# Kernel tuning notes

Measured on AMD Instinct MI355X. Metric: run time of the kernel, lower is better.

Reference implementation:

```python
import jax, jax.numpy as jnp
import numpy as np

G, N, E = 4, 50000, 400000   # subgraphs, nodes/graph, edges/graph
D = 128                      # num_node_feat = num_g_hid = out_g_ch
L = 3                        # num_layers
NE, AH = 8, 64               # num_expert, num_att_hid
FE = 8                       # num_edge_feat (unused by GIN conv)
LN_EPS = 1e-5


def setup_inputs() -> dict:
    key = jax.random.key(0)
    ks = jax.random.split(key, 12)
    s = 1.0 / np.sqrt(D)
    inp = {
        "decomp_x": jax.random.normal(ks[0], (G, N, D), dtype=jnp.float32),
        "decomp_edge_index": jax.random.randint(ks[1], (G, 2, E), 0, N, dtype=jnp.int32),
        "decomp_edge_attr": jax.random.normal(ks[2], (G, E, FE), dtype=jnp.float32),
        # GIN MLP params per layer: Linear(D,D) -> ReLU -> Linear(D,D), stored [in,out]
        "Ws1": jax.random.uniform(ks[3], (L, D, D), jnp.float32, -s, s),
        "bs1": jax.random.uniform(ks[4], (L, D), jnp.float32, -s, s),
        "Ws2": jax.random.uniform(ks[5], (L, D, D), jnp.float32, -s, s),
        "bs2": jax.random.uniform(ks[6], (L, D), jnp.float32, -s, s),
        "ln_g": jnp.ones((L, D), jnp.float32),
        "ln_b": jnp.zeros((L, D), jnp.float32),
        # Attention: w1 [n_hidden, v_hidden], w2 [n_expert, n_hidden]
        "att_w1": jax.random.uniform(ks[7], (AH, D), jnp.float32, -1.0 / np.sqrt(D), 1.0 / np.sqrt(D)),
        "att_w2": jax.random.uniform(ks[8], (NE, AH), jnp.float32, -1.0 / np.sqrt(AH), 1.0 / np.sqrt(AH)),
    }
    return inp


def _layer_norm(h, g, b):
    mu = jnp.mean(h, axis=-1, keepdims=True)
    var = jnp.var(h, axis=-1, keepdims=True)
    return (h - mu) * jax.lax.rsqrt(var + LN_EPS) * g + b


def _gin_graph(x, edge_index, Ws1, bs1, Ws2, bs2, ln_g, ln_b):
    # x: [N, D]; edge_index: [2, E] (src, dst)
    src, dst = edge_index[0], edge_index[1]
    for l in range(L):
        identity = x
        # GINConv (eps=0): MLP(x_i + sum_{j->i} x_j)
        agg = jax.ops.segment_sum(x[src], dst, num_segments=N)  # gather+scatter
        h = x + agg
        h = jnp.maximum(h @ Ws1[l] + bs1[l], 0.0) @ Ws2[l] + bs2[l]
        if l < L - 1:
            h = h + identity  # same dims, no projection
        x = _layer_norm(h, ln_g[l], ln_b[l])
    return jnp.sum(x, axis=0)  # [D] graph readout (sum over nodes)


def reference(decomp_x, decomp_edge_index, decomp_edge_attr,
              Ws1, bs1, Ws2, bs2, ln_g, ln_b, att_w1, att_w2):
    # edge_attr is unused by the GIN conv path (only NaN-checked in torch)
    g = jax.vmap(_gin_graph, in_axes=(0, 0, None, None, None, None, None, None))(
        decomp_x, decomp_edge_index, Ws1, bs1, Ws2, bs2, ln_g, ln_b)  # [G, D]
    # Attention pooling over subgraph vectors
    support = jnp.tanh(att_w1 @ g.T)                 # [AH, G]
    att = jax.nn.softmax(att_w2 @ support, axis=1)   # [NE, G]
    pooled = att @ g                                 # [NE, D]
    return pooled.reshape(1, NE * D)                 # [1, NE*D]
```

## Files before the change

### kernel.cpp

```cpp
#include <hip/hip_runtime.h>
#include <math.h>

#define G 4
#define NN 50000
#define EE 400000
#define D 128
#define LN_EPS 1e-5f
#define BPG 782
#define NB 4
#define BSZ 12500
#define M (NN * NB)
#define SM 200008
#define CH 2048
#define NCH ((M + CH - 1) / CH)

typedef _Float16 f16;
typedef _Float16 f16x4 __attribute__((ext_vector_type(4)));
typedef _Float16 f16x8 __attribute__((ext_vector_type(8)));
typedef float f32x4 __attribute__((ext_vector_type(4)));


__global__ __launch_bounds__(256) void hist_kernel(const int* __restrict__ ei, int* __restrict__ deg) {
    int idx = blockIdx.x * 256 + threadIdx.x;
    if (idx >= G * EE) return;
    int g = idx / EE, e = idx - g * EE;
    int src = ei[g * 2 * EE + e];
    int dst = ei[g * 2 * EE + EE + e];
    int b = src / BSZ;
    atomicAdd(&deg[g * M + dst * NB + b], 1);
}


__global__ __launch_bounds__(256) void scan_part(const int* __restrict__ deg, int* __restrict__ E,
                                                 int* __restrict__ part) {
    int b = blockIdx.x;
    int g = b / NCH, c = b - g * NCH;
    int t = threadIdx.x;
    int base = c * CH + t * 8;
    const int* dg = deg + g * M;
    int v[8];
    int s = 0;
#pragma unroll
    for (int j = 0; j < 8; ++j) {
        int i = base + j;
        v[j] = (i < M) ? dg[i] : 0;
        s += v[j];
    }
    __shared__ int sums[256];
    sums[t] = s;
    __syncthreads();
    for (int off = 1; off < 256; off <<= 1) {
        int x = (t >= off) ? sums[t - off] : 0;
        __syncthreads();
        sums[t] += x;
        __syncthreads();
    }
    int run = (t == 0) ? 0 : sums[t - 1];
    int* Eg = E + g * SM;
#pragma unroll
    for (int j = 0; j < 8; ++j) {
        int i = base + j;
        if (i < M) Eg[1 + i] = run;
        run += v[j];
    }
    if (t == 255) part[g * NCH + c] = sums[255];
    if (c == 0 && t == 0) Eg[0] = 0;
}

__global__ __launch_bounds__(128) void scan_tops(int* __restrict__ part) {
    int g = blockIdx.x, t = threadIdx.x;
    __shared__ int s[128];
    int v = (t < NCH) ? part[g * NCH + t] : 0;
    s[t] = v;
    __syncthreads();
    for (int off = 1; off < 128; off <<= 1) {
        int x = (t >= off) ? s[t - off] : 0;
        __syncthreads();
        s[t] += x;
        __syncthreads();
    }
    if (t < NCH) part[g * NCH + t] = s[t] - v;
}

__global__ __launch_bounds__(256) void scan_add(const int* __restrict__ part, int* __restrict__ E) {
    int b = blockIdx.x;
    int g = b / NCH, c = b - g * NCH;
    int off = part[g * NCH + c];
    if (off == 0) return;
    int t = threadIdx.x;
    int base = c * CH + t * 8;
    int* Eg = E + g * SM + 1;
#pragma unroll
    for (int j = 0; j < 8; ++j) {
        int i = base + j;
        if (i < M) Eg[i] += off;
    }
}

__global__ __launch_bounds__(256) void place_kernel(const int* __restrict__ ei, int* __restrict__ E,
                                                    int* __restrict__ csr_src) {
    int idx = blockIdx.x * 256 + threadIdx.x;
    if (idx >= G * EE) return;
    int g = idx / EE, e = idx - g * EE;
    int src = ei[g * 2 * EE + e];
    int dst = ei[g * 2 * EE + EE + e];
    int b = src / BSZ;
    int pos = atomicAdd(&E[g * SM + 1 + dst * NB + b], 1);
    csr_src[g * EE + pos] = src;
}


__global__ __launch_bounds__(256) void cast_x_kernel(const float* __restrict__ x, f16* __restrict__ o) {
    int i = blockIdx.x * 256 + threadIdx.x;
    float4 v = ((const float4*)x)[i];
    f16x4 h = {(f16)v.x, (f16)v.y, (f16)v.z, (f16)v.w};
    ((f16x4*)o)[i] = h;
}

__global__ __launch_bounds__(256) void cast_w_kernel(const float* __restrict__ Ws1, const float* __restrict__ Ws2,
                                                     f16* __restrict__ Wt) {
    int e = blockIdx.x * 256 + threadIdx.x;
    int mat = e >> 14, r = (e >> 7) & 127, c = e & 127;
    const float* src = (mat < 3) ? (Ws1 + mat * 16384) : (Ws2 + (mat - 3) * 16384);
    Wt[e] = (f16)src[c * 128 + r];
}


__global__ __launch_bounds__(256, 4) void gin_layer(
    const f16* __restrict__ Xin, f16* __restrict__ Xout,
    const int* __restrict__ E, const int* __restrict__ csr_src,
    const f16* __restrict__ W1t, const f16* __restrict__ W2t,
    const float* __restrict__ b1, const float* __restrict__ b2,
    const float* __restrict__ lng, const float* __restrict__ lnb,
    int has_res, int do_read, float* __restrict__ gvec)
{
    __shared__ f16 A[64][136];
    __shared__ f16 ID[64][136];
    __shared__ float colsum[128];

    int t = threadIdx.x;
    int slot = blockIdx.x & 7;
    int gi = blockIdx.x >> 3;
    int g = slot & 3;
    int bb = (slot >> 2) * 391 + gi;
    int nrow0 = bb * 64;
    long row0 = (long)g * NN + nrow0;
    int valid = min(64, NN - nrow0);

    if (do_read) {
        if (t < 128) colsum[t] = 0.f;
        __syncthreads();
    }

    {
        int grp = t >> 4, lane = t & 15;
        const int* Eg = E + g * SM;
        const int* srcs = csr_src + (long)g * EE;
        long gbase = (long)g * NN * 16;
        const f16x8* Xv = (const f16x8*)Xin;

        float acc[4][8];
        int bnd[4][5];
#pragma unroll
        for (int i = 0; i < 4; ++i) {
            int r = grp * 4 + i;
            if (r < valid) {
                int n = nrow0 + r;
                f16x8 self = Xv[(row0 + r) * 16 + lane];
                if (has_res) *(f16x8*)&ID[r][lane * 8] = self;
#pragma unroll
                for (int j = 0; j < 8; ++j) acc[i][j] = (float)self[j];
                int4 b4 = *(const int4*)&Eg[n * NB];
                bnd[i][0] = b4.x; bnd[i][1] = b4.y; bnd[i][2] = b4.z; bnd[i][3] = b4.w;
                bnd[i][4] = Eg[n * NB + 4];
            } else {
#pragma unroll
                for (int j = 0; j < 8; ++j) acc[i][j] = 0.f;
#pragma unroll
                for (int j = 0; j < 5; ++j) bnd[i][j] = 0;
            }
        }

#pragma unroll
        for (int b = 0; b < NB; ++b) {
#pragma unroll
            for (int i = 0; i < 4; ++i) {
                int s0 = bnd[i][b], s1 = bnd[i][b + 1];
                int k = s0;
                for (; k + 1 < s1; k += 2) {
                    f16x8 v0 = Xv[gbase + (long)srcs[k] * 16 + lane];
                    f16x8 v1 = Xv[gbase + (long)srcs[k + 1] * 16 + lane];
#pragma unroll
                    for (int j = 0; j < 8; ++j) acc[i][j] += (float)v0[j] + (float)v1[j];
                }
                if (k < s1) {
                    f16x8 v0 = Xv[gbase + (long)srcs[k] * 16 + lane];
#pragma unroll
                    for (int j = 0; j < 8; ++j) acc[i][j] += (float)v0[j];
                }
            }
        }

#pragma unroll
        for (int i = 0; i < 4; ++i) {
            int r = grp * 4 + i;
            f16x8 o;
#pragma unroll
            for (int j = 0; j < 8; ++j) o[j] = (f16)acc[i][j];
            *(f16x8*)&A[r][lane * 8] = o;
        }
    }

    int w = t >> 6, l = t & 63, q = l >> 4, cl = l & 15;
    int mrow = w * 16 + cl;

    const f16x8* Wb1 = (const f16x8*)W1t + (cl * 16 + q);
    f32x4 acc[8];
#pragma unroll
    for (int ns = 0; ns < 8; ++ns) acc[ns] = (f32x4){0.f, 0.f, 0.f, 0.f};
#pragma unroll
    for (int kc = 0; kc < 4; ++kc) {
        f16x8 a = *(const f16x8*)&A[mrow][kc * 32 + q * 8];
#pragma unroll
        for (int ns = 0; ns < 8; ++ns) {
            f16x8 b = Wb1[ns * 256 + kc * 4];
            acc[ns] = __builtin_amdgcn_mfma_f32_16x16x32_f16(a, b, acc[ns], 0, 0, 0);
        }
    }

#pragma unroll
    for (int ns = 0; ns < 8; ++ns) {
        float bv = b1[ns * 16 + cl];
#pragma unroll
        for (int r = 0; r < 4; ++r) {
            float v = fmaxf(acc[ns][r] + bv, 0.f);
            A[w * 16 + q * 4 + r][ns * 16 + cl] = (f16)v;
        }
    }

    const f16x8* Wb2 = (const f16x8*)W2t + (cl * 16 + q);
    f32x4 acc2[8];
#pragma unroll
    for (int ns = 0; ns < 8; ++ns) acc2[ns] = (f32x4){0.f, 0.f, 0.f, 0.f};
#pragma unroll
    for (int kc = 0; kc < 4; ++kc) {
        f16x8 a = *(const f16x8*)&A[mrow][kc * 32 + q * 8];
#pragma unroll
        for (int ns = 0; ns < 8; ++ns) {
            f16x8 b = Wb2[ns * 256 + kc * 4];
            acc2[ns] = __builtin_amdgcn_mfma_f32_16x16x32_f16(a, b, acc2[ns], 0, 0, 0);
        }
    }

    float o[8][4];
    float gm[8], gb[8];
#pragma unroll
    for (int ns = 0; ns < 8; ++ns) {
        int col = ns * 16 + cl;
        float b2v = b2[col];
        gm[ns] = lng[col];
        gb[ns] = lnb[col];
#pragma unroll
        for (int r = 0; r < 4; ++r) o[ns][r] = acc2[ns][r] + b2v;
    }
    if (has_res) {
#pragma unroll
        for (int r = 0; r < 4; ++r) {
            int lr = w * 16 + q * 4 + r;
#pragma unroll
            for (int ns = 0; ns < 8; ++ns) o[ns][r] += (float)ID[lr][ns * 16 + cl];
        }
    }

#pragma unroll
    for (int r = 0; r < 4; ++r) {
        float s1 = 0.f, s2 = 0.f;
#pragma unroll
        for (int ns = 0; ns < 8; ++ns) { s1 += o[ns][r]; s2 += o[ns][r] * o[ns][r]; }
        s1 += __shfl_xor(s1, 1); s2 += __shfl_xor(s2, 1);
        s1 += __shfl_xor(s1, 2); s2 += __shfl_xor(s2, 2);
        s1 += __shfl_xor(s1, 4); s2 += __shfl_xor(s2, 4);
        s1 += __shfl_xor(s1, 8); s2 += __shfl_xor(s2, 8);
        float mean = s1 * (1.f / 128.f);
        float var = s2 * (1.f / 128.f) - mean * mean;
        float rstd = rsqrtf(var + LN_EPS);
#pragma unroll
        for (int ns = 0; ns < 8; ++ns) o[ns][r] = (o[ns][r] - mean) * rstd * gm[ns] + gb[ns];
    }

    if (!do_read) {
#pragma unroll
        for (int ns = 0; ns < 8; ++ns)
#pragma unroll
            for (int r = 0; r < 4; ++r)
                A[w * 16 + q * 4 + r][ns * 16 + cl] = (f16)o[ns][r];
        int rr = w * 16 + (l >> 2), seg = l & 3;
        if (rr < valid) {
            f16* dst = Xout + (row0 + rr) * 128 + seg * 32;
            const f16* srcp = &A[rr][seg * 32];
            *(f16x8*)(dst)      = *(const f16x8*)(srcp);
            *(f16x8*)(dst + 8)  = *(const f16x8*)(srcp + 8);
            *(f16x8*)(dst + 16) = *(const f16x8*)(srcp + 16);
            *(f16x8*)(dst + 24) = *(const f16x8*)(srcp + 24);
        }
    } else {
#pragma unroll
        for (int ns = 0; ns < 8; ++ns) {
            float v = 0.f;
#pragma unroll
            for (int r = 0; r < 4; ++r) {
                int lr = w * 16 + q * 4 + r;
                if (lr < valid) v += o[ns][r];
            }
            v += __shfl_xor(v, 16);
            v += __shfl_xor(v, 32);
            if (l < 16) atomicAdd(&colsum[ns * 16 + cl], v);
        }
        __syncthreads();
        if (t < 128) atomicAdd(&gvec[g * 128 + t], colsum[t]);
    }
}


__global__ __launch_bounds__(256) void att_kernel(const float* __restrict__ gvec, const float* __restrict__ w1,
                                                  const float* __restrict__ w2, float* __restrict__ out) {
    __shared__ float sup[64][4];
    __shared__ float att[8][4];
    int t = threadIdx.x;
    int ah = t >> 2, gg = t & 3;
    float d = 0.f;
    for (int k = 0; k < 128; ++k) d += w1[ah * 128 + k] * gvec[gg * 128 + k];
    sup[ah][gg] = tanhf(d);
    __syncthreads();
    if (t < 32) {
        int ne = t >> 2, g2 = t & 3;
        float sc = 0.f;
        for (int k = 0; k < 64; ++k) sc += w2[ne * 64 + k] * sup[k][g2];
        att[ne][g2] = sc;
    }
    __syncthreads();
    if (t < 8) {
        float m = fmaxf(fmaxf(att[t][0], att[t][1]), fmaxf(att[t][2], att[t][3]));
        float e0 = expf(att[t][0] - m), e1 = expf(att[t][1] - m);
        float e2 = expf(att[t][2] - m), e3 = expf(att[t][3] - m);
        float inv = 1.f / (e0 + e1 + e2 + e3);
        att[t][0] = e0 * inv; att[t][1] = e1 * inv; att[t][2] = e2 * inv; att[t][3] = e3 * inv;
    }
    __syncthreads();
    for (int o = t; o < 1024; o += 256) {
        int ne = o >> 7, dd = o & 127;
        float v = 0.f;
        for (int g2 = 0; g2 < 4; ++g2) v += att[ne][g2] * gvec[g2 * 128 + dd];
        out[o] = v;
    }
}


extern "C" void kernel_launch(void* const* d_in, const int* in_sizes, int n_in,
                              void* d_out, int out_size, void* d_ws, size_t ws_size,
                              hipStream_t stream) {
    const float* x   = (const float*)d_in[0];
    const int*   ei  = (const int*)d_in[1];
    const float* Ws1 = (const float*)d_in[3];
    const float* bs1 = (const float*)d_in[4];
    const float* Ws2 = (const float*)d_in[5];
    const float* bs2 = (const float*)d_in[6];
    const float* lng = (const float*)d_in[7];
    const float* lnb = (const float*)d_in[8];
    const float* aw1 = (const float*)d_in[9];
    const float* aw2 = (const float*)d_in[10];

    char* ws = (char*)d_ws;
    f16*   XA       = (f16*)(ws);
    f16*   XB       = (f16*)(ws + 51200000);
    int*   csr_src  = (int*)(ws + 102400000);
    int*   E        = (int*)(ws + 108800000);
    f16*   Wt       = (f16*)(ws + 112000256);
    float* gvec     = (float*)(ws + 112196864);
    int*   part     = (int*)(ws + 112198912);
    int*   deg      = (int*)(ws + 51200000);

    hipMemsetAsync(deg, 0, G * M * sizeof(int), stream);
    hipMemsetAsync(gvec, 0, G * D * sizeof(float), stream);

    hist_kernel<<<(G * EE + 255) / 256, 256, 0, stream>>>(ei, deg);
    scan_part<<<G * NCH, 256, 0, stream>>>(deg, E, part);
    scan_tops<<<G, 128, 0, stream>>>(part);
    scan_add<<<G * NCH, 256, 0, stream>>>(part, E);
    place_kernel<<<(G * EE + 255) / 256, 256, 0, stream>>>(ei, E, csr_src);

    cast_x_kernel<<<(G * NN * D / 4) / 256, 256, 0, stream>>>(x, XA);
    cast_w_kernel<<<(6 * D * D) / 256, 256, 0, stream>>>(Ws1, Ws2, Wt);

    f16* Xcur = XA;
    f16* Xnxt = XB;
    for (int l = 0; l < 3; ++l) {
        gin_layer<<<G * BPG, 256, 0, stream>>>(Xcur, Xnxt, E, csr_src,
                                               Wt + l * D * D, Wt + (3 + l) * D * D,
                                               bs1 + l * D, bs2 + l * D,
                                               lng + l * D, lnb + l * D,
                                               (l < 2) ? 1 : 0, (l == 2) ? 1 : 0, gvec);
        f16* tmp = Xcur; Xcur = Xnxt; Xnxt = tmp;
    }
    att_kernel<<<1, 256, 0, stream>>>(gvec, aw1, aw2, (float*)d_out);
}
```

Measured before the change: 973.1 us.

## Use plain per-node CSR, drop source bucketing and shared identity tile

```diff
diff --git a/kernel.cpp b/kernel.cpp
--- a/kernel.cpp
+++ b/kernel.cpp
@@ -7,12 +7,9 @@
 #define D 128
 #define LN_EPS 1e-5f
 #define BPG 782
-#define NB 4
-#define BSZ 12500
-#define M (NN * NB)
-#define SM 200008
+#define SM 50008
 #define CH 2048
-#define NCH ((M + CH - 1) / CH)
+#define NCH ((NN + CH - 1) / CH)
 
 typedef _Float16 f16;
 typedef _Float16 f16x4 __attribute__((ext_vector_type(4)));
@@ -24,10 +21,8 @@
     int idx = blockIdx.x * 256 + threadIdx.x;
     if (idx >= G * EE) return;
     int g = idx / EE, e = idx - g * EE;
-    int src = ei[g * 2 * EE + e];
     int dst = ei[g * 2 * EE + EE + e];
-    int b = src / BSZ;
-    atomicAdd(&deg[g * M + dst * NB + b], 1);
+    atomicAdd(&deg[g * NN + dst], 1);
 }
 
 
@@ -37,13 +32,13 @@
     int g = b / NCH, c = b - g * NCH;
     int t = threadIdx.x;
     int base = c * CH + t * 8;
-    const int* dg = deg + g * M;
+    const int* dg = deg + g * NN;
     int v[8];
     int s = 0;
 #pragma unroll
     for (int j = 0; j < 8; ++j) {
         int i = base + j;
-        v[j] = (i < M) ? dg[i] : 0;
+        v[j] = (i < NN) ? dg[i] : 0;
         s += v[j];
     }
     __shared__ int sums[256];
@@ -60,7 +55,7 @@
 #pragma unroll
     for (int j = 0; j < 8; ++j) {
         int i = base + j;
-        if (i < M) Eg[1 + i] = run;
+        if (i < NN) Eg[1 + i] = run;
         run += v[j];
     }
     if (t == 255) part[g * NCH + c] = sums[255];
@@ -93,7 +88,7 @@
 #pragma unroll
     for (int j = 0; j < 8; ++j) {
         int i = base + j;
-        if (i < M) Eg[i] += off;
+        if (i < NN) Eg[i] += off;
     }
 }
 
@@ -104,8 +99,7 @@
     int g = idx / EE, e = idx - g * EE;
     int src = ei[g * 2 * EE + e];
     int dst = ei[g * 2 * EE + EE + e];
-    int b = src / BSZ;
-    int pos = atomicAdd(&E[g * SM + 1 + dst * NB + b], 1);
+    int pos = atomicAdd(&E[g * SM + 1 + dst], 1);
     csr_src[g * EE + pos] = src;
 }
 
@@ -126,7 +120,7 @@
 }
 
 
-__global__ __launch_bounds__(256, 4) void gin_layer(
+__global__ __launch_bounds__(256, 8) void gin_layer(
     const f16* __restrict__ Xin, f16* __restrict__ Xout,
     const int* __restrict__ E, const int* __restrict__ csr_src,
     const f16* __restrict__ W1t, const f16* __restrict__ W2t,
@@ -135,7 +129,6 @@
     int has_res, int do_read, float* __restrict__ gvec)
 {
     __shared__ f16 A[64][136];
-    __shared__ f16 ID[64][136];
     __shared__ float colsum[128];
 
     int t = threadIdx.x;
@@ -154,60 +147,40 @@
 
     {
         int grp = t >> 4, lane = t & 15;
-        const int* Eg = E + g * SM;
+        const int* rs = E + g * SM;
         const int* srcs = csr_src + (long)g * EE;
         long gbase = (long)g * NN * 16;
         const f16x8* Xv = (const f16x8*)Xin;
-
-        float acc[4][8];
-        int bnd[4][5];
 #pragma unroll
         for (int i = 0; i < 4; ++i) {
             int r = grp * 4 + i;
             if (r < valid) {
                 int n = nrow0 + r;
                 f16x8 self = Xv[(row0 + r) * 16 + lane];
-                if (has_res) *(f16x8*)&ID[r][lane * 8] = self;
-#pragma unroll
-                for (int j = 0; j < 8; ++j) acc[i][j] = (float)self[j];
-                int4 b4 = *(const int4*)&Eg[n * NB];
-                bnd[i][0] = b4.x; bnd[i][1] = b4.y; bnd[i][2] = b4.z; bnd[i][3] = b4.w;
-                bnd[i][4] = Eg[n * NB + 4];
-            } else {
-#pragma unroll
-                for (int j = 0; j < 8; ++j) acc[i][j] = 0.f;
-#pragma unroll
-                for (int j = 0; j < 5; ++j) bnd[i][j] = 0;
-            }
-        }
-
-#pragma unroll
-        for (int b = 0; b < NB; ++b) {
-#pragma unroll
-            for (int i = 0; i < 4; ++i) {
-                int s0 = bnd[i][b], s1 = bnd[i][b + 1];
+                float acc[8];
+#pragma unroll
+                for (int j = 0; j < 8; ++j) acc[j] = (float)self[j];
+                int s0 = rs[n], s1 = rs[n + 1];
                 int k = s0;
                 for (; k + 1 < s1; k += 2) {
                     f16x8 v0 = Xv[gbase + (long)srcs[k] * 16 + lane];
                     f16x8 v1 = Xv[gbase + (long)srcs[k + 1] * 16 + lane];
 #pragma unroll
-                    for (int j = 0; j < 8; ++j) acc[i][j] += (float)v0[j] + (float)v1[j];
+                    for (int j = 0; j < 8; ++j) acc[j] += (float)v0[j] + (float)v1[j];
                 }
                 if (k < s1) {
                     f16x8 v0 = Xv[gbase + (long)srcs[k] * 16 + lane];
 #pragma unroll
-                    for (int j = 0; j < 8; ++j) acc[i][j] += (float)v0[j];
+                    for (int j = 0; j < 8; ++j) acc[j] += (float)v0[j];
                 }
+                f16x8 o;
+#pragma unroll
+                for (int j = 0; j < 8; ++j) o[j] = (f16)acc[j];
+                *(f16x8*)&A[r][lane * 8] = o;
+            } else {
+                f16x8 z = {0, 0, 0, 0, 0, 0, 0, 0};
+                *(f16x8*)&A[r][lane * 8] = z;
             }
-        }
-
-#pragma unroll
-        for (int i = 0; i < 4; ++i) {
-            int r = grp * 4 + i;
-            f16x8 o;
-#pragma unroll
-            for (int j = 0; j < 8; ++j) o[j] = (f16)acc[i][j];
-            *(f16x8*)&A[r][lane * 8] = o;
         }
     }
 
@@ -267,8 +240,11 @@
 #pragma unroll
         for (int r = 0; r < 4; ++r) {
             int lr = w * 16 + q * 4 + r;
-#pragma unroll
-            for (int ns = 0; ns < 8; ++ns) o[ns][r] += (float)ID[lr][ns * 16 + cl];
+            if (lr < valid) {
+                const f16* xr = Xin + (row0 + lr) * 128 + cl;
+#pragma unroll
+                for (int ns = 0; ns < 8; ++ns) o[ns][r] += (float)xr[ns * 16];
+            }
         }
     }
 
@@ -375,12 +351,12 @@
     f16*   XB       = (f16*)(ws + 51200000);
     int*   csr_src  = (int*)(ws + 102400000);
     int*   E        = (int*)(ws + 108800000);
-    f16*   Wt       = (f16*)(ws + 112000256);
-    float* gvec     = (float*)(ws + 112196864);
-    int*   part     = (int*)(ws + 112198912);
+    f16*   Wt       = (f16*)(ws + 109600256);
+    float* gvec     = (float*)(ws + 109796864);
+    int*   part     = (int*)(ws + 109798912);
     int*   deg      = (int*)(ws + 51200000);
 
-    hipMemsetAsync(deg, 0, G * M * sizeof(int), stream);
+    hipMemsetAsync(deg, 0, G * NN * sizeof(int), stream);
     hipMemsetAsync(gvec, 0, G * D * sizeof(float), stream);
 
     hist_kernel<<<(G * EE + 255) / 256, 256, 0, stream>>>(ei, deg);
```

Result: faster. 911.8 us (-6.3%).
